# Performance work log

Measured on AMD Instinct MI355X. Metric: run time of the kernel, lower is better.

Reference implementation:

```python
import jax, jax.numpy as jnp
import numpy as np

A = 25                 # anchors per cell (kmeans anchors)
FEAT_STRIDE = 16
PRE_NMS = 6000
POST_NMS = 300
NMS_THRESH = 0.7
MIN_SIZE = 16.0
H_IMG, W_IMG = 608, 1024

_CIN  = [3, 64, 64, 128, 128, 256, 256, 256, 512, 512, 512, 512, 512]
_COUT = [64, 64, 128, 128, 256, 256, 256, 512, 512, 512, 512, 512, 512]
_POOL_AFTER = {1, 3, 6, 9}  # 2x2 maxpool after these conv idxs (last VGG pool deleted)


def _base_anchors():
    scales = np.exp(np.linspace(np.log(2.0), np.log(64.0), A))
    ratios = np.exp(np.linspace(np.log(0.25), np.log(4.0), A))
    size = FEAT_STRIDE * scales
    w = size / np.sqrt(ratios)
    h = w * ratios
    c = (FEAT_STRIDE - 1) / 2.0
    return np.stack([c - (w - 1) / 2, c - (h - 1) / 2,
                     c + (w - 1) / 2, c + (h - 1) / 2], 1).astype(np.float32)

_BASE = jnp.asarray(_base_anchors())  # [A,4]


def _conv(x, w, b, pad):
    y = jax.lax.conv_general_dilated(x, w, (1, 1), [(pad, pad), (pad, pad)],
                                     dimension_numbers=('NCHW', 'OIHW', 'NCHW'))
    return y + b[None, :, None, None]


def _maxpool2(x):
    return jax.lax.reduce_window(x, -jnp.inf, jax.lax.max,
                                 (1, 1, 2, 2), (1, 1, 2, 2), 'VALID')


def _nms_keep(boxes, thresh):
    # boxes sorted by descending score; greedy NMS with the +1 area convention
    x1, y1, x2, y2 = boxes[:, 0], boxes[:, 1], boxes[:, 2], boxes[:, 3]
    areas = (x2 - x1 + 1) * (y2 - y1 + 1)
    xx1 = jnp.maximum(x1[:, None], x1[None, :]); yy1 = jnp.maximum(y1[:, None], y1[None, :])
    xx2 = jnp.minimum(x2[:, None], x2[None, :]); yy2 = jnp.minimum(y2[:, None], y2[None, :])
    inter = jnp.maximum(xx2 - xx1 + 1, 0) * jnp.maximum(yy2 - yy1 + 1, 0)
    iou = inter / (areas[:, None] + areas[None, :] - inter)
    n = boxes.shape[0]

    def body(valid, i):
        keep_i = valid[i]
        sup = keep_i & (iou[i] > thresh)
        sup = sup.at[i].set(False)
        return valid & ~sup, keep_i

    _, keep = jax.lax.scan(body, jnp.ones((n,), bool), jnp.arange(n))
    return keep


def _forward(im_data, im_info, vgg_w, vgg_b, wrpn, brpn, wscr, bscr, wbox, bbx):
    x = im_data
    for i in range(13):
        x = jax.nn.relu(_conv(x, vgg_w[i], vgg_b[i], 1))
        if i in _POOL_AFTER:
            x = _maxpool2(x)
    feat = x                                         # [1,512,H,W], stride 16
    rc = jax.nn.relu(_conv(feat, wrpn, brpn, 1))
    score = _conv(rc, wscr, bscr, 0)                 # [1,2A,H,W]
    bbox = _conv(rc, wbox, bbx, 0)                   # [1,4A,H,W]
    B, _, H, W = score.shape
    # reshape_layer(score,2) -> softmax(dim=1) -> reshape back; fg = channels A:2A
    prob = jax.nn.softmax(score.reshape(B, 2, A, H, W), axis=1)
    fg = prob[0, 1]                                  # [A,H,W]
    scores = jnp.transpose(fg, (1, 2, 0)).reshape(-1)          # [H*W*A]
    deltas = jnp.transpose(bbox[0], (1, 2, 0)).reshape(-1, 4)  # [H*W*A,4]
    # anchor grid
    sx = jnp.arange(W, dtype=jnp.float32) * FEAT_STRIDE
    sy = jnp.arange(H, dtype=jnp.float32) * FEAT_STRIDE
    sxg, syg = jnp.meshgrid(sx, sy)                  # [H,W]
    shift = jnp.stack([sxg, syg, sxg, syg], -1)      # [H,W,4]
    anchors = (_BASE[None, None] + shift[:, :, None, :]).reshape(-1, 4)
    # bbox_transform_inv
    wa = anchors[:, 2] - anchors[:, 0] + 1
    ha = anchors[:, 3] - anchors[:, 1] + 1
    cxa = anchors[:, 0] + 0.5 * wa
    cya = anchors[:, 1] + 0.5 * ha
    cx = deltas[:, 0] * wa + cxa
    cy = deltas[:, 1] * ha + cya
    pw = jnp.exp(deltas[:, 2]) * wa
    ph = jnp.exp(deltas[:, 3]) * ha
    # clip to image
    x1 = jnp.clip(cx - 0.5 * pw, 0, im_info[0, 1] - 1)
    y1 = jnp.clip(cy - 0.5 * ph, 0, im_info[0, 0] - 1)
    x2 = jnp.clip(cx + 0.5 * pw, 0, im_info[0, 1] - 1)
    y2 = jnp.clip(cy + 0.5 * ph, 0, im_info[0, 0] - 1)
    boxes = jnp.stack([x1, y1, x2, y2], 1)
    # min-size filter (mask instead of drop, for static shapes)
    ms = MIN_SIZE * im_info[0, 2]
    big = ((x2 - x1 + 1) >= ms) & ((y2 - y1 + 1) >= ms)
    scr = jnp.where(big, scores, -1e9)
    # pre-NMS top-k
    top_i = jax.lax.top_k(jax.lax.stop_gradient(scr), PRE_NMS)[1]
    boxes_k = boxes[top_i]
    scores_k = scr[top_i]
    keep = _nms_keep(jax.lax.stop_gradient(boxes_k), NMS_THRESH)
    keep = keep & (jax.lax.stop_gradient(scores_k) > -1e8)
    idx = jnp.argsort(jnp.where(keep, 0, 1))[:POST_NMS]  # stable: kept first, score order
    ok = keep[idx].astype(boxes.dtype)
    rois = jnp.concatenate([jnp.zeros((POST_NMS, 1), boxes.dtype),
                            boxes_k[idx] * ok[:, None],
                            (scores_k[idx] * ok)[:, None]], 1)  # [POST_NMS, 6]
    return feat, rois


def setup_inputs():
    key = jax.random.key(0)
    ks = iter(jax.random.split(key, 40))
    inp = {}
    for i in range(13):
        std = float(np.sqrt(2.0 / (_CIN[i] * 9)))
        inp['w%d' % i] = jax.random.normal(next(ks), (_COUT[i], _CIN[i], 3, 3), jnp.float32) * std
        inp['b%d' % i] = jnp.zeros((_COUT[i],), jnp.float32)
    inp['wrpn'] = jax.random.normal(next(ks), (512, 512, 3, 3), jnp.float32) * 0.025
    inp['brpn'] = jnp.zeros((512,), jnp.float32)
    inp['wscr'] = jax.random.normal(next(ks), (2 * A, 512, 1, 1), jnp.float32) * 0.025
    inp['bscr'] = jnp.zeros((2 * A,), jnp.float32)
    inp['wbox'] = jax.random.normal(next(ks), (4 * A, 512, 1, 1), jnp.float32) * 0.01
    inp['bbx'] = jnp.zeros((4 * A,), jnp.float32)
    inp['im_data'] = jax.random.normal(next(ks), (1, 3, H_IMG, W_IMG), jnp.float32)
    inp['im_info'] = jnp.array([[float(H_IMG), float(W_IMG), 1.0]], jnp.float32)
    return inp


def reference(w0, b0, w1, b1, w2, b2, w3, b3, w4, b4, w5, b5, w6, b6, w7, b7,
              w8, b8, w9, b9, w10, b10, w11, b11, w12, b12,
              wrpn, brpn, wscr, bscr, wbox, bbx, im_data, im_info):
    vgg_w = [w0, w1, w2, w3, w4, w5, w6, w7, w8, w9, w10, w11, w12]
    vgg_b = [b0, b1, b2, b3, b4, b5, b6, b7, b8, b9, b10, b11, b12]
    return _forward(im_data, im_info, vgg_w, vgg_b, wrpn, brpn, wscr, bscr, wbox, bbx)
```

## Files before the change

kernel.cpp:

```cpp
#include <hip/hip_runtime.h>
#include <math.h>

namespace {

constexpr int kNA    = 25;
constexpr int kPre   = 6000;
constexpr int kPost  = 300;
constexpr int kSortN = 8192;
constexpr int kWords = (kPre + 63) / 64;

template<int TW, int TH, int COT, bool POOLOUT>
__global__ __launch_bounds__(256) void conv_full(
    const float* __restrict__ in, const float* __restrict__ wgt,
    const float* __restrict__ bias, float* __restrict__ out,
    int Cin, int H, int W, int outStride)
{
  constexpr int CIT = 4;
  constexpr int PG  = TH * (TW / 4);
  constexpr int CG  = 256 / PG;
  constexpr int CPT = COT / CG;
  constexpr int IN_ELEMS = CIT * (TH + 2) * (TW + 2);
  constexpr int W_ELEMS  = COT * CIT * 9;

  __shared__ float s_in[CIT][TH + 2][TW + 4];
  __shared__ float s_w[COT][CIT * 9 + 1];
  __shared__ float s_pool[POOLOUT ? CG : 1][POOLOUT ? TH : 1][POOLOUT ? TW + 1 : 1];

  const int t   = threadIdx.x;
  const int cg  = t & (CG - 1);
  const int pg  = t / CG;
  const int py  = pg / (TW / 4);
  const int px  = (pg % (TW / 4)) * 4;
  const int bx  = blockIdx.x * TW;
  const int by  = blockIdx.y * TH;
  const int co0 = blockIdx.z * COT;
  const int col = cg * CPT;

  double acc[CPT][4];
#pragma unroll
  for (int o = 0; o < CPT; ++o)
#pragma unroll
    for (int q = 0; q < 4; ++q) acc[o][q] = 0.0;

  for (int ci0 = 0; ci0 < Cin; ci0 += CIT) {
    for (int e = t; e < IN_ELEMS; e += 256) {
      int cc  = e / ((TH + 2) * (TW + 2));
      int rem = e - cc * ((TH + 2) * (TW + 2));
      int r   = rem / (TW + 2);
      int c   = rem - r * (TW + 2);
      int ci = ci0 + cc, y = by - 1 + r, gx = bx - 1 + c;
      float v = 0.f;
      if (ci < Cin && (unsigned)y < (unsigned)H && (unsigned)gx < (unsigned)W)
        v = in[((size_t)ci * H + y) * W + gx];
      s_in[cc][r][c] = v;
    }
    for (int e = t; e < W_ELEMS; e += 256) {
      int o   = e / (CIT * 9);
      int rem = e - o * (CIT * 9);
      int cc  = rem / 9;
      int ci  = ci0 + cc;
      float v = (ci < Cin) ? wgt[((size_t)(co0 + o) * Cin + ci) * 9 + (rem - cc * 9)] : 0.f;
      s_w[o][rem] = v;
    }
    __syncthreads();

#pragma unroll
    for (int cc = 0; cc < CIT; ++cc) {
      float vin[3][6];
#pragma unroll
      for (int r = 0; r < 3; ++r)
#pragma unroll
        for (int c = 0; c < 6; ++c) vin[r][c] = s_in[cc][py + r][px + c];
#pragma unroll
      for (int o = 0; o < CPT; ++o) {
#pragma unroll
        for (int r = 0; r < 3; ++r)
#pragma unroll
          for (int k = 0; k < 3; ++k) {
            double wv = (double)s_w[col + o][cc * 9 + r * 3 + k];
#pragma unroll
            for (int q = 0; q < 4; ++q)
              acc[o][q] = fma(wv, (double)vin[r][k + q], acc[o][q]);
          }
      }
    }
    __syncthreads();
  }

  if (!POOLOUT) {
    const int y = by + py;
#pragma unroll
    for (int o = 0; o < CPT; ++o) {
      int co = co0 + col + o;
      double bv = (double)bias[co];
#pragma unroll
      for (int q = 0; q < 4; ++q) {
        int gx = bx + px + q;
        if (y < H && gx < W) {
          double v = acc[o][q] + bv;
          out[((size_t)co * H + y) * outStride + gx] = v > 0.0 ? (float)v : 0.f;
        }
      }
    }
  } else {
    const int prow = pg / (TW / 2);
    const int pcol = pg % (TW / 2);
#pragma unroll
    for (int o = 0; o < CPT; ++o) {
      int co = co0 + col + o;
      double bv = (double)bias[co];
#pragma unroll
      for (int q = 0; q < 4; ++q) {
        double v = acc[o][q] + bv;
        s_pool[cg][py][px + q] = v > 0.0 ? (float)v : 0.f;
      }
      __syncthreads();
      float v = fmaxf(fmaxf(s_pool[cg][2 * prow][2 * pcol],     s_pool[cg][2 * prow][2 * pcol + 1]),
                      fmaxf(s_pool[cg][2 * prow + 1][2 * pcol], s_pool[cg][2 * prow + 1][2 * pcol + 1]));
      int gy  = by / 2 + prow;
      int gxc = bx + 2 * pcol;
      if (gy < H / 2 && gxc < W)
        out[((size_t)co * (H / 2) + gy) * outStride + (gxc >> 1)] = v;
      __syncthreads();
    }
  }
}

__global__ void probe_kernel(float* __restrict__ rois, float val)
{
  if (threadIdx.x == 0 && blockIdx.x == 0) rois[0] = val;
}

__global__ void clear_u32(unsigned int* __restrict__ p, int n)
{
  int i = blockIdx.x * 256 + threadIdx.x;
  if (i < n) p[i] = 0u;
}

__global__ __launch_bounds__(256) void head1x1(
    const float* __restrict__ rc,
    const float* __restrict__ wscr, const float* __restrict__ bscr,
    const float* __restrict__ wbox, const float* __restrict__ bbx,
    float* __restrict__ score, float* __restrict__ bbox, int npix)
{
  int pix = blockIdx.x * 256 + threadIdx.x;
  int co  = blockIdx.y;
  const float* wrow; float bv; float* outp;
  if (co < 50) { wrow = wscr + (size_t)co * 512; bv = bscr[co]; outp = score + (size_t)co * npix; }
  else { int c2 = co - 50; wrow = wbox + (size_t)c2 * 512; bv = bbx[c2]; outp = bbox + (size_t)c2 * npix; }
  if (pix >= npix) return;
  double acc = 0.0;
  for (int k = 0; k < 512; ++k)
    acc = fma((double)wrow[k], (double)rc[(size_t)k * npix + pix], acc);
  outp[pix] = (float)(acc + (double)bv);
}

__device__ inline unsigned orderable(float f) {
  unsigned b = __float_as_uint(f);
  return (b & 0x80000000u) ? ~b : (b | 0x80000000u);
}

__global__ void decode_kernel(
    const float* __restrict__ score, const float* __restrict__ bbox,
    const float* __restrict__ iminfo,
    float* __restrict__ scr, float* __restrict__ boxes,
    unsigned int* __restrict__ hist1, int H, int W)
{
#pragma clang fp contract(off)
  int n = blockIdx.x * 256 + threadIdx.x;
  int npix = H * W;
  if (n >= npix * kNA) return;
  int a   = n % kNA;
  int pix = n / kNA;
  int x = pix % W, y = pix / W;

  float s0 = score[(size_t)a * npix + pix];
  float s1 = score[(size_t)(kNA + a) * npix + pix];
  float m = fmaxf(s0, s1);
  float e0 = expf(s0 - m), e1 = expf(s1 - m);
  float fg = e1 / (e0 + e1);

  float d0 = bbox[(size_t)(a * 4 + 0) * npix + pix];
  float d1 = bbox[(size_t)(a * 4 + 1) * npix + pix];
  float d2 = bbox[(size_t)(a * 4 + 2) * npix + pix];
  float d3 = bbox[(size_t)(a * 4 + 3) * npix + pix];

  double ls = log(2.0), le = log(64.0);
  double sc = (a == 24) ? 64.0 : exp(ls + a * ((le - ls) / 24.0));
  double lr = log(0.25), lre = log(4.0);
  double rr = (a == 24) ? 4.0 : exp(lr + a * ((lre - lr) / 24.0));
  double size = 16.0 * sc;
  double wd = size / sqrt(rr);
  double hd = wd * rr;
  float ax1 = (float)(7.5 - (wd - 1.0) / 2.0);
  float ay1 = (float)(7.5 - (hd - 1.0) / 2.0);
  float ax2 = (float)(7.5 + (wd - 1.0) / 2.0);
  float ay2 = (float)(7.5 + (hd - 1.0) / 2.0);

  float sx = (float)x * 16.0f, sy = (float)y * 16.0f;
  float x1a = ax1 + sx, y1a = ay1 + sy, x2a = ax2 + sx, y2a = ay2 + sy;

  float wa = x2a - x1a + 1.0f;
  float ha = y2a - y1a + 1.0f;
  float cxa = x1a + 0.5f * wa;
  float cya = y1a + 0.5f * ha;
  float cx = d0 * wa + cxa;
  float cy = d1 * ha + cya;
  float pw = expf(d2) * wa;
  float ph = expf(d3) * ha;

  float Wm1 = iminfo[1] - 1.0f, Hm1 = iminfo[0] - 1.0f;
  float x1 = fminf(fmaxf(cx - 0.5f * pw, 0.f), Wm1);
  float y1 = fminf(fmaxf(cy - 0.5f * ph, 0.f), Hm1);
  float x2 = fminf(fmaxf(cx + 0.5f * pw, 0.f), Wm1);
  float y2 = fminf(fmaxf(cy + 0.5f * ph, 0.f), Hm1);

  float ms = 16.0f * iminfo[2];
  bool big = (x2 - x1 + 1.0f >= ms) && (y2 - y1 + 1.0f >= ms);
  float s = big ? fg : -1000000000.0f;

  scr[n] = s;
  boxes[(size_t)n * 4 + 0] = x1;
  boxes[(size_t)n * 4 + 1] = y1;
  boxes[(size_t)n * 4 + 2] = x2;
  boxes[(size_t)n * 4 + 3] = y2;
  atomicAdd(&hist1[orderable(s) >> 16], 1u);
}

__global__ __launch_bounds__(256) void find_bin1(
    const unsigned int* __restrict__ hist, int* __restrict__ meta)
{
  __shared__ unsigned part[256];
  int t = threadIdx.x;
  unsigned s = 0;
  for (int b = t * 256; b < t * 256 + 256; ++b) s += hist[b];
  part[t] = s;
  __syncthreads();
  if (t == 0) {
    unsigned cum = 0; int seg = 0;
    for (int p = 255; p >= 0; --p) {
      if (cum + part[p] >= (unsigned)kPre) { seg = p; break; }
      cum += part[p];
    }
    int B = seg * 256;
    for (int b = seg * 256 + 255; b >= seg * 256; --b) {
      if (cum + hist[b] >= (unsigned)kPre) { B = b; break; }
      cum += hist[b];
    }
    meta[0] = B;
    meta[1] = (int)cum;
  }
}

__global__ void pass2_hist(const float* __restrict__ scr, const int* __restrict__ meta,
                           unsigned int* __restrict__ hist2, int total)
{
  int n = blockIdx.x * 256 + threadIdx.x;
  if (n >= total) return;
  unsigned u = orderable(scr[n]);
  if ((int)(u >> 16) == meta[0]) atomicAdd(&hist2[u & 0xffffu], 1u);
}

__global__ __launch_bounds__(256) void find_bin2(
    const unsigned int* __restrict__ hist2, int* __restrict__ meta)
{
  __shared__ unsigned part[256];
  int t = threadIdx.x;
  unsigned s = 0;
  for (int b = t * 256; b < t * 256 + 256; ++b) s += hist2[b];
  part[t] = s;
  __syncthreads();
  if (t == 0) {
    unsigned need = (unsigned)(kPre - meta[1]);
    unsigned cum = 0; int seg = 0;
    for (int p = 255; p >= 0; --p) {
      if (cum + part[p] >= need) { seg = p; break; }
      cum += part[p];
    }
    int B = seg * 256;
    for (int b = seg * 256 + 255; b >= seg * 256; --b) {
      if (cum + hist2[b] >= need) { B = b; break; }
      cum += hist2[b];
    }
    meta[2] = B;
    meta[3] = meta[1] + (int)cum;
    meta[4] = kPre - (meta[1] + (int)cum);
  }
}

__global__ void collect_strict(const float* __restrict__ scr, int* __restrict__ meta,
                               unsigned long long* __restrict__ cand, int total)
{
  int n = blockIdx.x * 256 + threadIdx.x;
  if (n >= total) return;
  unsigned u = orderable(scr[n]);
  unsigned u_th = (((unsigned)meta[0]) << 16) | (unsigned)meta[2];
  if (u > u_th) {
    int pos = atomicAdd(&meta[5], 1);
    if (pos < kPre)
      cand[pos] = (((unsigned long long)(~u)) << 32) | (unsigned)n;
  }
}

__global__ __launch_bounds__(256) void collect_ties(
    const float* __restrict__ scr, const int* __restrict__ meta,
    unsigned long long* __restrict__ cand, int total)
{
  __shared__ int ps[256];
  __shared__ int s_taken;
  int t = threadIdx.x;
  if (t == 0) s_taken = 0;
  unsigned u_th = (((unsigned)meta[0]) << 16) | (unsigned)meta[2];
  int base_pos = meta[3];
  int needT    = meta[4];
  __syncthreads();
  for (int base = 0; base < total; base += 256) {
    int n = base + t;
    int flag = (n < total) && (orderable(scr[n]) == u_th);
    ps[t] = flag;
    __syncthreads();
    for (int off = 1; off < 256; off <<= 1) {
      int v = (t >= off) ? ps[t - off] : 0;
      __syncthreads();
      ps[t] += v;
      __syncthreads();
    }
    int rank = s_taken + ps[t] - flag;
    if (flag && rank < needT)
      cand[base_pos + rank] = (((unsigned long long)(~u_th)) << 32) | (unsigned)n;
    __syncthreads();
    if (t == 0) s_taken += ps[255];
    __syncthreads();
  }
}

__global__ __launch_bounds__(256) void sort_topk_global(
    unsigned long long* __restrict__ cand,
    const float* __restrict__ scr, const float* __restrict__ boxes,
    float* __restrict__ scores_k, float* __restrict__ boxes_k)
{
  int t = threadIdx.x;
  for (int i = kPre + t; i < kSortN; i += 256) cand[i] = ~0ull;
  __syncthreads();
  for (unsigned k = 2; k <= (unsigned)kSortN; k <<= 1) {
    for (unsigned j = k >> 1; j > 0; j >>= 1) {
      for (int i = t; i < kSortN; i += 256) {
        int ixj = i ^ (int)j;
        if (ixj > i) {
          unsigned long long a = cand[i], b = cand[ixj];
          bool up = ((i & (int)k) == 0);
          if ((a > b) == up) { cand[i] = b; cand[ixj] = a; }
        }
      }
      __syncthreads();
    }
  }
  for (int jj = t; jj < kPre; jj += 256) {
    int idx = (int)(cand[jj] & 0xffffffffull);
    scores_k[jj] = scr[idx];
    ((float4*)boxes_k)[jj] = ((const float4*)boxes)[idx];
  }
}

__global__ void nms_mask_kernel(const float* __restrict__ boxes_k,
                                unsigned long long* __restrict__ mask)
{
#pragma clang fp contract(off)
  __shared__ float4 cb[64];
  int t  = threadIdx.x;
  int cbk = blockIdx.x, rbk = blockIdx.y;
  int j0 = cbk * 64;
  if (j0 + t < kPre) cb[t] = ((const float4*)boxes_k)[j0 + t];
  __syncthreads();
  int i = rbk * 64 + t;
  if (i >= kPre) return;
  float4 bi = ((const float4*)boxes_k)[i];
  float ai = (bi.z - bi.x + 1.0f) * (bi.w - bi.y + 1.0f);
  unsigned long long bits = 0;
  int jmax = min(64, kPre - j0);
  for (int jj = 0; jj < jmax; ++jj) {
    int j = j0 + jj;
    if (j == i) continue;
    float4 bj = cb[jj];
    float xx1 = fmaxf(bi.x, bj.x), yy1 = fmaxf(bi.y, bj.y);
    float xx2 = fminf(bi.z, bj.z), yy2 = fminf(bi.w, bj.w);
    float inter = fmaxf(xx2 - xx1 + 1.0f, 0.f) * fmaxf(yy2 - yy1 + 1.0f, 0.f);
    float aj = (bj.z - bj.x + 1.0f) * (bj.w - bj.y + 1.0f);
    float iou = inter / (ai + aj - inter);
    if (iou > 0.7f) bits |= 1ull << jj;
  }
  mask[(size_t)i * kWords + cbk] = bits;
}

__global__ void nms_scan_kernel(const unsigned long long* __restrict__ mask,
                                int* __restrict__ keep)
{
  __shared__ int s_alive;
  int t = threadIdx.x;
  unsigned long long rem = 0;
  for (int i = 0; i < kPre; ++i) {
    if (t == (i >> 6)) s_alive = !((rem >> (i & 63)) & 1ull);
    __syncthreads();
    int alive = s_alive;
    if (alive && t < kWords) rem |= mask[(size_t)i * kWords + t];
    if (t == 0) keep[i] = alive;
    __syncthreads();
  }
}

__global__ __launch_bounds__(256) void make_rois(
    const int* __restrict__ keep, const float* __restrict__ scores_k,
    const float* __restrict__ boxes_k, float* __restrict__ rois)
{
  __shared__ int part[256];
  int t = threadIdx.x;
  unsigned mask24 = 0;
  int cnt = 0;
#pragma unroll
  for (int e = 0; e < 24; ++e) {
    int i = t * 24 + e;
    int k = (i < kPre) && keep[i] && (scores_k[i] > -100000000.0f);
    mask24 |= (unsigned)k << e;
    cnt += k;
  }
  part[t] = cnt;
  __syncthreads();
  for (int off = 1; off < 256; off <<= 1) {
    int v = (t >= off) ? part[t - off] : 0;
    __syncthreads();
    part[t] += v;
    __syncthreads();
  }
  int total = part[255];
  int pos = part[t] - cnt;
#pragma unroll
  for (int e = 0; e < 24; ++e) {
    if ((mask24 >> e) & 1u) {
      if (pos < kPost) {
        int i = t * 24 + e;
        float4 b = ((const float4*)boxes_k)[i];
        rois[(size_t)pos * 6 + 0] = 0.f;
        rois[(size_t)pos * 6 + 1] = b.x;
        rois[(size_t)pos * 6 + 2] = b.y;
        rois[(size_t)pos * 6 + 3] = b.z;
        rois[(size_t)pos * 6 + 4] = b.w;
        rois[(size_t)pos * 6 + 5] = scores_k[i];
      }
      ++pos;
    }
  }
  for (int r = total + t; r < kPost; r += 256)
    for (int c = 0; c < 6; ++c) rois[(size_t)r * 6 + c] = 0.f;
}

}

extern "C" void kernel_launch(void* const* d_in, const int* in_sizes, int n_in,
                              void* d_out, int out_size, void* d_ws, size_t ws_size,
                              hipStream_t stream)
{
  const float* w[13];
  const float* b[13];
  for (int i = 0; i < 13; ++i) { w[i] = (const float*)d_in[2 * i]; b[i] = (const float*)d_in[2 * i + 1]; }
  const float* wrpn = (const float*)d_in[26];
  const float* brpn = (const float*)d_in[27];
  const float* wscr = (const float*)d_in[28];
  const float* bscr = (const float*)d_in[29];
  const float* wbox = (const float*)d_in[30];
  const float* bbx  = (const float*)d_in[31];
  const float* im   = (const float*)d_in[32];
  const float* info = (const float*)d_in[33];

  float* feat = (float*)d_out;
  float* rois = feat + 1245184;

  {
    int wsMB = (int)(ws_size >> 20); if (wsMB > 500) wsMB = 500;
    probe_kernel<<<1, 64, 0, stream>>>(rois, 4096.0f + 8.0f * (float)wsMB);
  }

  const size_t FN = 39845888;
  const size_t XN = 9961472;
  const size_t CN = 4980736;
  float* F = (float*)d_ws;
  float* X = F + FN;
  float* C = X + XN;
  int*   meta = (int*)(C + CN);
  size_t needed = (size_t)((char*)(meta + 64) - (char*)d_ws);
  if (ws_size < needed) return;

  float* scoreb   = C;
  float* bboxb    = C + 121600;
  float* scr      = C + 364800;
  float* boxes    = C + 425600;
  float* scores_k = C + 668800;
  float* boxes_k  = C + 674800;
  int*   keep     = (int*)(C + 698800);
  unsigned* hist  = (unsigned*)(C + 704800);
  unsigned long long* cand = (unsigned long long*)(C + 835872);
  unsigned long long* maskbuf = (unsigned long long*)(C + 852256);

  conv_full<32,8,32,false><<<dim3(32,76,2),  256, 0, stream>>>(im, w[0],  b[0],  F,    3, 608, 1024, 1024);
  conv_full<32,8,32,true ><<<dim3(32,76,2),  256, 0, stream>>>(F,  w[1],  b[1],  X,   64, 608, 1024,  512);
  conv_full<32,8,32,false><<<dim3(16,38,4),  256, 0, stream>>>(X,  w[2],  b[2],  F,   64, 304,  512,  512);
  conv_full<32,8,32,true ><<<dim3(16,38,4),  256, 0, stream>>>(F,  w[3],  b[3],  C,  128, 304,  512,  256);
  conv_full<32,8,32,false><<<dim3(8,19,8),   256, 0, stream>>>(C,  w[4],  b[4],  X,  128, 152,  256,  256);
  conv_full<32,8,32,false><<<dim3(8,19,8),   256, 0, stream>>>(X,  w[5],  b[5],  F,  256, 152,  256,  256);
  conv_full<32,8,32,true ><<<dim3(8,19,8),   256, 0, stream>>>(F,  w[6],  b[6],  X,  256, 152,  256,  128);
  conv_full<32,8,16,false><<<dim3(4,10,32),  256, 0, stream>>>(X,  w[7],  b[7],  F,  256,  76,  128,  128);
  conv_full<32,8,16,false><<<dim3(4,10,32),  256, 0, stream>>>(F,  w[8],  b[8],  X,  512,  76,  128,  128);
  conv_full<32,8,16,true ><<<dim3(4,10,32),  256, 0, stream>>>(X,  w[9],  b[9],  F,  512,  76,  128,   64);
  conv_full<16,8,8,false><<<dim3(4,5,64),    256, 0, stream>>>(F,  w[10], b[10], X,  512,  38,   64,   64);
  conv_full<16,8,8,false><<<dim3(4,5,64),    256, 0, stream>>>(X,  w[11], b[11], F,  512,  38,   64,   64);
  conv_full<16,8,8,false><<<dim3(4,5,64),    256, 0, stream>>>(F,  w[12], b[12], feat, 512, 38,  64,   64);
  conv_full<16,8,8,false><<<dim3(4,5,64),    256, 0, stream>>>(feat, wrpn, brpn, X,  512,  38,   64,   64);

  head1x1<<<dim3(10, 150), 256, 0, stream>>>(X, wscr, bscr, wbox, bbx, scoreb, bboxb, 2432);
  clear_u32<<<(131072 + 255) / 256, 256, 0, stream>>>(hist, 131072);
  clear_u32<<<1, 64, 0, stream>>>((unsigned*)meta, 64);
  decode_kernel<<<238, 256, 0, stream>>>(scoreb, bboxb, info, scr, boxes, hist, 38, 64);
  find_bin1<<<1, 256, 0, stream>>>(hist, meta);
  pass2_hist<<<238, 256, 0, stream>>>(scr, meta, hist + 65536, 60800);
  find_bin2<<<1, 256, 0, stream>>>(hist + 65536, meta);
  collect_strict<<<238, 256, 0, stream>>>(scr, meta, cand, 60800);
  collect_ties<<<1, 256, 0, stream>>>(scr, meta, cand, 60800);
  sort_topk_global<<<1, 256, 0, stream>>>(cand, scr, boxes, scores_k, boxes_k);

  nms_mask_kernel<<<dim3(kWords, kWords), 64, 0, stream>>>(boxes_k, maskbuf);
  nms_scan_kernel<<<1, 128, 0, stream>>>(maskbuf, keep);
  make_rois<<<1, 256, 0, stream>>>(keep, scores_k, boxes_k, rois);
}
```

Measured before the change: 15.50 ms.

## Split top-k bitonic sort across LDS blocks and use wave-shuffle NMS scan

Replaces the single-block bitonic sort over global memory with two 4096-element shared-memory sorts, a cross-chunk compare step and a shared-memory merge, followed by a separate parallel gather kernel. The NMS scan now runs as a single 64-lane wavefront that passes the alive bit with a shuffle instead of two block barriers per box, each lane holding two mask words. The conv inner loop also converts input values to double once when loading them rather than at every FMA. This targets the serial barrier-heavy sort and scan, at the cost of extra kernel launches.

```diff
diff --git a/kernel.cpp b/kernel.cpp
--- a/kernel.cpp
+++ b/kernel.cpp
@@ -66,11 +66,11 @@
 
 #pragma unroll
     for (int cc = 0; cc < CIT; ++cc) {
-      float vin[3][6];
+      double vin[3][6];
 #pragma unroll
       for (int r = 0; r < 3; ++r)
 #pragma unroll
-        for (int c = 0; c < 6; ++c) vin[r][c] = s_in[cc][py + r][px + c];
+        for (int c = 0; c < 6; ++c) vin[r][c] = (double)s_in[cc][py + r][px + c];
 #pragma unroll
       for (int o = 0; o < CPT; ++o) {
 #pragma unroll
@@ -80,7 +80,7 @@
             double wv = (double)s_w[col + o][cc * 9 + r * 3 + k];
 #pragma unroll
             for (int q = 0; q < 4; ++q)
-              acc[o][q] = fma(wv, (double)vin[r][k + q], acc[o][q]);
+              acc[o][q] = fma(wv, vin[r][k + q], acc[o][q]);
           }
       }
     }
@@ -334,32 +334,67 @@
   }
 }
 
-__global__ __launch_bounds__(256) void sort_topk_global(
-    unsigned long long* __restrict__ cand,
-    const float* __restrict__ scr, const float* __restrict__ boxes,
-    float* __restrict__ scores_k, float* __restrict__ boxes_k)
-{
+__global__ __launch_bounds__(256) void sort_chunk(unsigned long long* __restrict__ cand)
+{
+  __shared__ unsigned long long s[4096];
   int t = threadIdx.x;
-  for (int i = kPre + t; i < kSortN; i += 256) cand[i] = ~0ull;
-  __syncthreads();
-  for (unsigned k = 2; k <= (unsigned)kSortN; k <<= 1) {
+  int base = blockIdx.x * 4096;
+  for (int i = t; i < 4096; i += 256)
+    s[i] = (base + i < kPre) ? cand[base + i] : ~0ull;
+  __syncthreads();
+  for (unsigned k = 2; k <= 4096u; k <<= 1) {
     for (unsigned j = k >> 1; j > 0; j >>= 1) {
-      for (int i = t; i < kSortN; i += 256) {
+      for (int i = t; i < 4096; i += 256) {
         int ixj = i ^ (int)j;
         if (ixj > i) {
-          unsigned long long a = cand[i], b = cand[ixj];
-          bool up = ((i & (int)k) == 0);
-          if ((a > b) == up) { cand[i] = b; cand[ixj] = a; }
+          unsigned long long a = s[i], b = s[ixj];
+          bool up = (((unsigned)(base + i) & k) == 0);
+          if ((a > b) == up) { s[i] = b; s[ixj] = a; }
         }
       }
       __syncthreads();
     }
   }
-  for (int jj = t; jj < kPre; jj += 256) {
-    int idx = (int)(cand[jj] & 0xffffffffull);
-    scores_k[jj] = scr[idx];
-    ((float4*)boxes_k)[jj] = ((const float4*)boxes)[idx];
-  }
+  for (int i = t; i < 4096; i += 256) cand[base + i] = s[i];
+}
+
+__global__ void merge_cross(unsigned long long* __restrict__ cand)
+{
+  int i = blockIdx.x * 256 + threadIdx.x;
+  if (i >= 4096) return;
+  unsigned long long a = cand[i], b = cand[i + 4096];
+  if (a > b) { cand[i] = b; cand[i + 4096] = a; }
+}
+
+__global__ __launch_bounds__(256) void merge_finish(unsigned long long* __restrict__ cand)
+{
+  __shared__ unsigned long long s[4096];
+  int t = threadIdx.x;
+  int base = blockIdx.x * 4096;
+  for (int i = t; i < 4096; i += 256) s[i] = cand[base + i];
+  __syncthreads();
+  for (unsigned j = 2048; j > 0; j >>= 1) {
+    for (int i = t; i < 4096; i += 256) {
+      int ixj = i ^ (int)j;
+      if (ixj > i) {
+        unsigned long long a = s[i], b = s[ixj];
+        if (a > b) { s[i] = b; s[ixj] = a; }
+      }
+    }
+    __syncthreads();
+  }
+  for (int i = t; i < 4096; i += 256) cand[base + i] = s[i];
+}
+
+__global__ void gather_topk(const unsigned long long* __restrict__ cand,
+                            const float* __restrict__ scr, const float* __restrict__ boxes,
+                            float* __restrict__ scores_k, float* __restrict__ boxes_k)
+{
+  int j = blockIdx.x * 256 + threadIdx.x;
+  if (j >= kPre) return;
+  int idx = (int)(cand[j] & 0xffffffffull);
+  scores_k[j] = scr[idx];
+  ((float4*)boxes_k)[j] = ((const float4*)boxes)[idx];
 }
 
 __global__ void nms_mask_kernel(const float* __restrict__ boxes_k,
@@ -392,19 +427,22 @@
   mask[(size_t)i * kWords + cbk] = bits;
 }
 
-__global__ void nms_scan_kernel(const unsigned long long* __restrict__ mask,
-                                int* __restrict__ keep)
-{
-  __shared__ int s_alive;
-  int t = threadIdx.x;
-  unsigned long long rem = 0;
+__global__ __launch_bounds__(64) void nms_scan_kernel(
+    const unsigned long long* __restrict__ mask, int* __restrict__ keep)
+{
+  int l = threadIdx.x;
+  unsigned long long rem0 = 0, rem1 = 0;
   for (int i = 0; i < kPre; ++i) {
-    if (t == (i >> 6)) s_alive = !((rem >> (i & 63)) & 1ull);
-    __syncthreads();
-    int alive = s_alive;
-    if (alive && t < kWords) rem |= mask[(size_t)i * kWords + t];
-    if (t == 0) keep[i] = alive;
-    __syncthreads();
+    int wi = i >> 6;
+    unsigned long long sel = (wi < 64) ? rem0 : rem1;
+    int owner = (wi < 64) ? wi : (wi - 64);
+    unsigned long long wv = __shfl(sel, owner, 64);
+    int alive = !((wv >> (i & 63)) & 1ull);
+    if (alive) {
+      rem0 |= mask[(size_t)i * kWords + l];
+      if (l < kWords - 64) rem1 |= mask[(size_t)i * kWords + 64 + l];
+    }
+    if (l == 0) keep[i] = alive;
   }
 }
 
@@ -524,9 +562,12 @@
   find_bin2<<<1, 256, 0, stream>>>(hist + 65536, meta);
   collect_strict<<<238, 256, 0, stream>>>(scr, meta, cand, 60800);
   collect_ties<<<1, 256, 0, stream>>>(scr, meta, cand, 60800);
-  sort_topk_global<<<1, 256, 0, stream>>>(cand, scr, boxes, scores_k, boxes_k);
+  sort_chunk<<<2, 256, 0, stream>>>(cand);
+  merge_cross<<<16, 256, 0, stream>>>(cand);
+  merge_finish<<<2, 256, 0, stream>>>(cand);
+  gather_topk<<<(kPre + 255) / 256, 256, 0, stream>>>(cand, scr, boxes, scores_k, boxes_k);
 
   nms_mask_kernel<<<dim3(kWords, kWords), 64, 0, stream>>>(boxes_k, maskbuf);
-  nms_scan_kernel<<<1, 128, 0, stream>>>(maskbuf, keep);
+  nms_scan_kernel<<<1, 64, 0, stream>>>(maskbuf, keep);
   make_rois<<<1, 256, 0, stream>>>(keep, scores_k, boxes_k, rois);
 }
```

Result: faster. 14.76 ms (-4.8%).
